# Optimization experiments

Measured on AMD Instinct MI355X. Metric: run time of the kernel, lower is better.

## Reference

```python
import jax, jax.numpy as jnp
import numpy as np

LEAKY_SLOPE = 0.2

def _xavier(key, shape, gain=1.414):
    a = gain * np.sqrt(6.0 / (shape[0] + shape[1]))
    return jax.random.uniform(key, shape, minval=-a, maxval=a, dtype=jnp.float32)

C_IN, HID = 64, 128
S_SCALES = [25, 12, 5]
T_SCALES = [64, 32, 16]

def setup_inputs() -> dict:
    key = jax.random.key(0)
    ks = jax.random.split(key, 32)
    B, T, J = 256, 64, 25
    d = {}
    d["src"] = jax.random.normal(ks[0], (B, C_IN, T, J), dtype=jnp.float32)
    d["W"] = _xavier(ks[1], (C_IN, HID))
    for i in range(3):
        d[f"as_src{i}"] = _xavier(ks[2 + i], (HID, 1))
        d[f"as_dst{i}"] = _xavier(ks[5 + i], (HID, 1))
        d[f"at_src{i}"] = _xavier(ks[8 + i], (HID, 1))
        d[f"at_dst{i}"] = _xavier(ks[11 + i], (HID, 1))
    # DiffPool assignment linears: in_features -> next_scale
    d["Wsp0"] = _xavier(ks[14], (C_IN, S_SCALES[1])); d["bsp0"] = jnp.zeros((S_SCALES[1],), jnp.float32)
    d["Wsp1"] = _xavier(ks[15], (C_IN, S_SCALES[2])); d["bsp1"] = jnp.zeros((S_SCALES[2],), jnp.float32)
    d["Wtp0"] = _xavier(ks[16], (C_IN, T_SCALES[1])); d["btp0"] = jnp.zeros((T_SCALES[1],), jnp.float32)
    d["Wtp1"] = _xavier(ks[17], (C_IN, T_SCALES[2])); d["btp1"] = jnp.zeros((T_SCALES[2],), jnp.float32)
    return d


def _gat_attn(emb, a_src, a_dst):
    # emb: [N, n, H]; additive GAT scores -> [N, n, n]
    s = emb @ a_src            # [N, n, 1]
    t = emb @ a_dst            # [N, n, 1]
    return jax.nn.leaky_relu(s + jnp.swapaxes(t, -1, -2), LEAKY_SLOPE)


def _diffpool(x, attn, Wp, bp):
    # assignment S = softmax(Linear(A @ X)) : [N, n, n_next]
    S = jax.nn.softmax((attn @ x) @ Wp + bp, axis=-1)
    x_next = jnp.einsum('bnk,bnc->bkc', S, x)
    return x_next, S


def _branch(x0, W, a_srcs, a_dsts, pool_params):
    n_scales = len(a_srcs)
    attns, pools = [], []
    x_cur = x0
    for i in range(n_scales):
        emb = x_cur @ W
        attns.append(_gat_attn(emb, a_srcs[i], a_dsts[i]))
        if i < n_scales - 1:
            Wp, bp = pool_params[i]
            x_cur, S = _diffpool(x_cur, attns[i], Wp, bp)
            pools.append(S)
    fusion = attns[0]
    for i in range(1, n_scales):
        S = pools[0]
        for j in range(1, i):
            S = S @ pools[j]
        fusion = fusion + S @ attns[i] @ jnp.swapaxes(S, -1, -2)
    # dropout is identity in eval mode
    return jax.nn.softmax(fusion, axis=-1)


def reference(src, W, as_src0, as_src1, as_src2, as_dst0, as_dst1, as_dst2,
              at_src0, at_src1, at_src2, at_dst0, at_dst1, at_dst2,
              Wsp0, bsp0, Wsp1, bsp1, Wtp0, btp0, Wtp1, btp1):
    B, C_in, T, J = src.shape
    x = jnp.transpose(src, (0, 2, 3, 1))              # [B, T, J, C]
    sp_x = x.reshape(B * T, J, C_in)                   # spatial graphs
    tp_x = jnp.transpose(x, (0, 2, 1, 3)).reshape(B * J, T, C_in)  # temporal graphs

    sa = _branch(sp_x, W, [as_src0, as_src1, as_src2], [as_dst0, as_dst1, as_dst2],
                 [(Wsp0, bsp0), (Wsp1, bsp1)])
    ta = _branch(tp_x, W, [at_src0, at_src1, at_src2], [at_dst0, at_dst1, at_dst2],
                 [(Wtp0, btp0), (Wtp1, btp1)])
    return sa.reshape(B, T, J, J), ta.reshape(B, J, T, T)
```

## Files before the change

### kernel.cpp

```cpp
#include <hip/hip_runtime.h>
#include <math.h>

constexpr float LEAKY = 0.2f;

__device__ __forceinline__ float4 ldf4(const float* p){ return *reinterpret_cast<const float4*>(p); }
__device__ __forceinline__ void stf4(float* p, float4 v){ *reinterpret_cast<float4*>(p) = v; }
__device__ __forceinline__ float dot4(float4 a, float4 b){ return a.x*b.x + a.y*b.y + a.z*b.z + a.w*b.w; }
__device__ __forceinline__ float4 fma4(float s, float4 b, float4 acc){
    acc.x += s*b.x; acc.y += s*b.y; acc.z += s*b.z; acc.w += s*b.w; return acc;
}
__device__ __forceinline__ float lrelu(float f){ return f > 0.f ? f : LEAKY*f; }
__device__ __forceinline__ float4 lrelu4(float s, float4 t){
    float4 r; r.x = lrelu(s+t.x); r.y = lrelu(s+t.y); r.z = lrelu(s+t.z); r.w = lrelu(s+t.w); return r;
}
__device__ __forceinline__ float vmax4(float4 v){ return fmaxf(fmaxf(v.x,v.y), fmaxf(v.z,v.w)); }
__device__ __forceinline__ float vsum4(float4 v){ return v.x+v.y+v.z+v.w; }
__device__ __forceinline__ float4 exp4(float4 a, float mx){
    float4 r; r.x = __expf(a.x-mx); r.y = __expf(a.y-mx); r.z = __expf(a.z-mx); r.w = __expf(a.w-mx); return r;
}

__global__ void prep_kernel(const float* __restrict__ W,
    const float* a0, const float* a1, const float* a2,  const float* a3,
    const float* a4, const float* a5, const float* a6,  const float* a7,
    const float* a8, const float* a9, const float* a10, const float* a11,
    const float* __restrict__ Wsp0, const float* __restrict__ Wsp1,
    const float* __restrict__ Wtp0, const float* __restrict__ Wtp1,
    float* __restrict__ ws)
{
    int blk = blockIdx.x, t = threadIdx.x;
    if (blk < 12) {
        const float* as[12] = {a0,a1,a2,a3,a4,a5,a6,a7,a8,a9,a10,a11};
        const float* a = as[blk];
        float s = 0.f;
        #pragma unroll
        for (int h = 0; h < 128; ++h) s += W[t*128 + h] * a[h];
        ws[blk*64 + t] = s;
    } else if (blk == 12) {
        for (int i = t; i < 768; i += 64) { int k = i >> 6, c = i & 63; ws[768 + i] = Wsp0[c*12 + k]; }
    } else if (blk == 13) {
        for (int i = t; i < 320; i += 64) { int k = i >> 6, c = i & 63; ws[1536 + i] = Wsp1[c*5 + k]; }
    } else if (blk == 14) {
        for (int i = t; i < 2048; i += 64) { int k = i >> 6, c = i & 63; ws[1856 + i] = Wtp0[c*32 + k]; }
    } else {
        for (int i = t; i < 1024; i += 64) { int k = i >> 6, c = i & 63; ws[3904 + i] = Wtp1[c*16 + k]; }
    }
}

__global__ __launch_bounds__(512, 4)
void temporal_kernel(const float* __restrict__ src, const float* __restrict__ wvec_g,
                     const float* __restrict__ Wp0, const float* __restrict__ b0,
                     const float* __restrict__ Wp1, const float* __restrict__ b1,
                     float* __restrict__ out, int nwg8)
{
    constexpr int NT = 512;
    constexpr int oA1 = 0;
    constexpr int oP1 = 1152;
    constexpr int oS1 = 1792;
    constexpr int oS0T = 2432;

    __shared__ __align__(16) float xr[4608];
    __shared__ __align__(16) float PR[2304];
    __shared__ __align__(16) float S0[2304];
    __shared__ __align__(16) float P01[1280];
    __shared__ __align__(16) float dv[256];
    __shared__ __align__(16) float sv[64], tv[64];
    __shared__ __align__(16) float s1v[32], t1v[32], ua[32], va[32];
    __shared__ __align__(16) float rx[16], rs[16];
    __shared__ __align__(16) float wv[384];

    const int tid = threadIdx.x;
    const int g = (blockIdx.x & 7) * nwg8 + (blockIdx.x >> 3);
    const int b = g / 25, inner = g - b*25;

    for (int i = tid; i < 384; i += NT) wv[i] = wvec_g[i];
    for (int i = tid; i < 4096; i += NT) {
        int c = i >> 6, r = i & 63;
        xr[r*68 + c] = src[((size_t)(b*64 + c)*64 + r)*25 + inner];
    }
    __syncthreads();

    if (tid < 64) {
        float acc[6] = {};
        #pragma unroll
        for (int c4 = 0; c4 < 16; ++c4) {
            float4 xv = ldf4(&xr[tid*68 + 4*c4]);
            #pragma unroll
            for (int d = 0; d < 6; ++d) acc[d] += dot4(xv, ldf4(&wv[d*64 + 4*c4]));
        }
        sv[tid] = acc[0]; tv[tid] = acc[1];
        dv[tid] = acc[2]; dv[64+tid] = acc[3]; dv[128+tid] = acc[4]; dv[192+tid] = acc[5];
    }
    for (int i = tid; i < 512; i += NT) {
        int p = i >> 3, k4 = i & 7;
        float4 acc = {0,0,0,0};
        #pragma unroll
        for (int c4 = 0; c4 < 16; ++c4) {
            float4 xv = ldf4(&xr[p*68 + 4*c4]);
            acc = fma4(xv.x, ldf4(&Wp0[(4*c4+0)*32 + 4*k4]), acc);
            acc = fma4(xv.y, ldf4(&Wp0[(4*c4+1)*32 + 4*k4]), acc);
            acc = fma4(xv.z, ldf4(&Wp0[(4*c4+2)*32 + 4*k4]), acc);
            acc = fma4(xv.w, ldf4(&Wp0[(4*c4+3)*32 + 4*k4]), acc);
        }
        stf4(&PR[p*36 + 4*k4], acc);
    }
    for (int i = tid; i < 256; i += NT) {
        int p = i >> 2, k4 = i & 3;
        float4 acc = {0,0,0,0};
        #pragma unroll
        for (int c4 = 0; c4 < 16; ++c4) {
            float4 xv = ldf4(&xr[p*68 + 4*c4]);
            acc = fma4(xv.x, ldf4(&Wp1[(4*c4+0)*16 + 4*k4]), acc);
            acc = fma4(xv.y, ldf4(&Wp1[(4*c4+1)*16 + 4*k4]), acc);
            acc = fma4(xv.z, ldf4(&Wp1[(4*c4+2)*16 + 4*k4]), acc);
            acc = fma4(xv.w, ldf4(&Wp1[(4*c4+3)*16 + 4*k4]), acc);
        }
        stf4(&P01[p*20 + 4*k4], acc);
    }
    __syncthreads();

    if (tid < 128) {
        int p0 = tid >> 2, k8 = tid & 3;
        float sp0 = sv[p0], sp1 = sv[p0+32];
        float4 a00 = ldf4(&b0[8*k8]), a01 = ldf4(&b0[8*k8 + 4]);
        float4 a10 = a00, a11 = a01;
        #pragma unroll
        for (int m4 = 0; m4 < 16; ++m4) {
            float4 tv4 = ldf4(&tv[4*m4]);
            float4 f0v = lrelu4(sp0, tv4);
            float4 f1v = lrelu4(sp1, tv4);
            const float* f0 = (const float*)&f0v;
            const float* f1 = (const float*)&f1v;
            #pragma unroll
            for (int j = 0; j < 4; ++j) {
                float4 pr0 = ldf4(&PR[(4*m4+j)*36 + 8*k8]);
                float4 pr1 = ldf4(&PR[(4*m4+j)*36 + 8*k8 + 4]);
                a00 = fma4(f0[j], pr0, a00); a01 = fma4(f0[j], pr1, a01);
                a10 = fma4(f1[j], pr0, a10); a11 = fma4(f1[j], pr1, a11);
            }
        }
        stf4(&S0[p0*36 + 8*k8], a00);      stf4(&S0[p0*36 + 8*k8 + 4], a01);
        stf4(&S0[(p0+32)*36 + 8*k8], a10); stf4(&S0[(p0+32)*36 + 8*k8 + 4], a11);
    }
    __syncthreads();

    {
        int p = tid >> 3, l = tid & 7;
        float4 v = ldf4(&S0[p*36 + 4*l]);
        float mx = vmax4(v);
        mx = fmaxf(mx, __shfl_xor(mx,1)); mx = fmaxf(mx, __shfl_xor(mx,2)); mx = fmaxf(mx, __shfl_xor(mx,4));
        v = exp4(v, mx);
        float sm = vsum4(v);
        sm += __shfl_xor(sm,1); sm += __shfl_xor(sm,2); sm += __shfl_xor(sm,4);
        float inv = 1.f/sm;
        v.x *= inv; v.y *= inv; v.z *= inv; v.w *= inv;
        stf4(&S0[p*36 + 4*l], v);
        xr[oS0T + (4*l+0)*68 + p] = v.x;
        xr[oS0T + (4*l+1)*68 + p] = v.y;
        xr[oS0T + (4*l+2)*68 + p] = v.z;
        xr[oS0T + (4*l+3)*68 + p] = v.w;
    }
    __syncthreads();

    if (tid < 64) {
        int k0 = tid >> 2, j4 = tid & 3;
        float4 acc0 = {0,0,0,0}, acc1 = {0,0,0,0};
        #pragma unroll
        for (int p4 = 0; p4 < 16; ++p4) {
            float4 s0 = ldf4(&xr[oS0T + k0*68 + 4*p4]);
            float4 s1 = ldf4(&xr[oS0T + (k0+16)*68 + 4*p4]);
            const float* f0 = (const float*)&s0;
            const float* f1 = (const float*)&s1;
            #pragma unroll
            for (int j = 0; j < 4; ++j) {
                float4 pv = ldf4(&P01[(4*p4+j)*20 + 4*j4]);
                acc0 = fma4(f0[j], pv, acc0);
                acc1 = fma4(f1[j], pv, acc1);
            }
        }
        stf4(&xr[oP1 + k0*20 + 4*j4], acc0);
        stf4(&xr[oP1 + (k0+16)*20 + 4*j4], acc1);
    } else if (tid < 192) {
        int i = tid - 64;
        int j = i >> 5, k = i & 31;
        const float* d = dv + j*64;
        float acc = 0.f;
        #pragma unroll
        for (int p4 = 0; p4 < 16; ++p4)
            acc += dot4(ldf4(&xr[oS0T + k*68 + 4*p4]), ldf4(&d[4*p4]));
        if (j == 0) s1v[k] = acc; else if (j == 1) t1v[k] = acc;
        else if (j == 2) ua[k] = acc; else va[k] = acc;
    }
    __syncthreads();

    for (int i = tid; i < 1024; i += NT) {
        int p = i >> 5, q = i & 31;
        xr[oA1 + p*36 + q] = lrelu(s1v[p] + t1v[q]);
    }
    __syncthreads();

    for (int i = tid; i < 128; i += NT) {
        int p = i >> 2, k4 = i & 3;
        float4 acc = ldf4(&b1[4*k4]);
        #pragma unroll
        for (int m = 0; m < 32; ++m) acc = fma4(xr[oA1 + p*36 + m], ldf4(&xr[oP1 + m*20 + 4*k4]), acc);
        stf4(&xr[oS1 + p*20 + 4*k4], acc);
    }
    __syncthreads();

    if (tid < 128) {
        int m = tid >> 2, l = tid & 3;
        float4 v = ldf4(&xr[oS1 + m*20 + 4*l]);
        float mx = vmax4(v);
        mx = fmaxf(mx, __shfl_xor(mx,1)); mx = fmaxf(mx, __shfl_xor(mx,2));
        v = exp4(v, mx);
        float sm = vsum4(v);
        sm += __shfl_xor(sm,1); sm += __shfl_xor(sm,2);
        float inv = 1.f/sm;
        v.x *= inv; v.y *= inv; v.z *= inv; v.w *= inv;
        stf4(&xr[oS1 + m*20 + 4*l], v);
    }
    __syncthreads();

    for (int k = tid; k < 16; k += NT) {
        float a = 0.f, c2 = 0.f;
        #pragma unroll
        for (int n = 0; n < 32; ++n) { float s1 = xr[oS1 + n*20 + k]; a += s1*ua[n]; c2 += s1*va[n]; }
        rx[k] = a; rs[k] = c2;
    }
    __syncthreads();

    {
        int m = tid >> 4, k = tid & 15;
        float rsk = rs[k];
        float acc = 0.f;
        #pragma unroll
        for (int j = 0; j < 16; ++j)
            acc += xr[oS1 + m*20 + j] * lrelu(rx[j] + rsk);
        xr[oP1 + m*20 + k] = acc;
    }
    __syncthreads();

    for (int i = tid; i < 1024; i += NT) {
        int m = i >> 5, n = i & 31;
        float acc = xr[oA1 + m*36 + n];
        #pragma unroll
        for (int j4 = 0; j4 < 4; ++j4)
            acc += dot4(ldf4(&xr[oP1 + m*20 + 4*j4]), ldf4(&xr[oS1 + n*20 + 4*j4]));
        xr[oA1 + m*36 + n] = acc;
    }
    __syncthreads();

    if (tid < 128) {
        int p0 = tid >> 2, k8 = tid & 3;
        float4 a00 = {0,0,0,0}, a01 = {0,0,0,0}, a10 = {0,0,0,0}, a11 = {0,0,0,0};
        #pragma unroll
        for (int m4 = 0; m4 < 8; ++m4) {
            float4 av0 = ldf4(&S0[p0*36 + 4*m4]);
            float4 av1 = ldf4(&S0[(p0+32)*36 + 4*m4]);
            const float* f0 = (const float*)&av0;
            const float* f1 = (const float*)&av1;
            #pragma unroll
            for (int j = 0; j < 4; ++j) {
                float4 b0v = ldf4(&xr[oA1 + (4*m4+j)*36 + 8*k8]);
                float4 b1v = ldf4(&xr[oA1 + (4*m4+j)*36 + 8*k8 + 4]);
                a00 = fma4(f0[j], b0v, a00); a01 = fma4(f0[j], b1v, a01);
                a10 = fma4(f1[j], b0v, a10); a11 = fma4(f1[j], b1v, a11);
            }
        }
        stf4(&PR[p0*36 + 8*k8], a00);      stf4(&PR[p0*36 + 8*k8 + 4], a01);
        stf4(&PR[(p0+32)*36 + 8*k8], a10); stf4(&PR[(p0+32)*36 + 8*k8 + 4], a11);
    }
    __syncthreads();

    if (tid < 256) {
        int p0 = tid >> 3, q8 = tid & 7;
        float sp0 = sv[p0], sp1 = sv[p0+32];
        float4 tq0 = ldf4(&tv[8*q8]), tq1 = ldf4(&tv[8*q8 + 4]);
        float4 a00 = lrelu4(sp0, tq0), a01 = lrelu4(sp0, tq1);
        float4 a10 = lrelu4(sp1, tq0), a11 = lrelu4(sp1, tq1);
        #pragma unroll
        for (int m4 = 0; m4 < 8; ++m4) {
            float4 av0 = ldf4(&PR[p0*36 + 4*m4]);
            float4 av1 = ldf4(&PR[(p0+32)*36 + 4*m4]);
            const float* f0 = (const float*)&av0;
            const float* f1 = (const float*)&av1;
            #pragma unroll
            for (int j = 0; j < 4; ++j) {
                float4 s0v = ldf4(&xr[oS0T + (4*m4+j)*68 + 8*q8]);
                float4 s1vv = ldf4(&xr[oS0T + (4*m4+j)*68 + 8*q8 + 4]);
                a00 = fma4(f0[j], s0v, a00); a01 = fma4(f0[j], s1vv, a01);
                a10 = fma4(f1[j], s0v, a10); a11 = fma4(f1[j], s1vv, a11);
            }
        }
        size_t base = (size_t)g * 4096;
        {
            float mx = fmaxf(vmax4(a00), vmax4(a01));
            mx = fmaxf(mx, __shfl_xor(mx,1)); mx = fmaxf(mx, __shfl_xor(mx,2)); mx = fmaxf(mx, __shfl_xor(mx,4));
            float4 e0 = exp4(a00, mx), e1 = exp4(a01, mx);
            float sm = vsum4(e0) + vsum4(e1);
            sm += __shfl_xor(sm,1); sm += __shfl_xor(sm,2); sm += __shfl_xor(sm,4);
            float inv = 1.f/sm;
            e0.x*=inv; e0.y*=inv; e0.z*=inv; e0.w*=inv;
            e1.x*=inv; e1.y*=inv; e1.z*=inv; e1.w*=inv;
            stf4(&out[base + (size_t)p0*64 + 8*q8], e0);
            stf4(&out[base + (size_t)p0*64 + 8*q8 + 4], e1);
        }
        {
            float mx = fmaxf(vmax4(a10), vmax4(a11));
            mx = fmaxf(mx, __shfl_xor(mx,1)); mx = fmaxf(mx, __shfl_xor(mx,2)); mx = fmaxf(mx, __shfl_xor(mx,4));
            float4 e0 = exp4(a10, mx), e1 = exp4(a11, mx);
            float sm = vsum4(e0) + vsum4(e1);
            sm += __shfl_xor(sm,1); sm += __shfl_xor(sm,2); sm += __shfl_xor(sm,4);
            float inv = 1.f/sm;
            e0.x*=inv; e0.y*=inv; e0.z*=inv; e0.w*=inv;
            e1.x*=inv; e1.y*=inv; e1.z*=inv; e1.w*=inv;
            stf4(&out[base + (size_t)(p0+32)*64 + 8*q8], e0);
            stf4(&out[base + (size_t)(p0+32)*64 + 8*q8 + 4], e1);
        }
    }
}

__global__ __launch_bounds__(256, 4)
void spatial_kernel(const float* __restrict__ src, const float* __restrict__ wvg,
                    const float* __restrict__ WpT0, const float* __restrict__ WpT1,
                    const float* __restrict__ b0, const float* __restrict__ b1,
                    float* __restrict__ out, int nwg8)
{
    __shared__ __align__(16) float Rx0[1700];
    __shared__ __align__(16) float RA0[700];
    __shared__ __align__(16) float RPR[816];
    __shared__ __align__(16) float RS0[500];
    __shared__ __align__(16) float sv[32], tv[32], ua[32], va[32], rxa[8], rsa[8];

    float* x0  = Rx0;
    float* A1  = Rx0;
    float* A1T = Rx0 + 240;
    float* P1T = Rx0 + 480;
    float* S1  = Rx0 + 540;
    float* T1  = Rx0 + 744;
    float* A0  = RA0;
    float* P0T = RPR;
    float* x1  = RPR;
    float* M1  = RPR;
    float* S0  = RS0;

    const int t = threadIdx.x;
    const int g = (blockIdx.x & 7) * nwg8 + (blockIdx.x >> 3);
    const int b = g >> 6, inner = g & 63;
    const float* srcb = src + (size_t)b*102400 + inner*25;

    for (int i = t; i < 400; i += 256) {
        int r = i % 25, c0 = (i / 25) << 2;
        float4 v;
        v.x = srcb[(c0+0)*1600 + r];
        v.y = srcb[(c0+1)*1600 + r];
        v.z = srcb[(c0+2)*1600 + r];
        v.w = srcb[(c0+3)*1600 + r];
        stf4(&x0[r*68 + c0], v);
    }
    __syncthreads();

    if (t < 50) {
        int which = t / 25, p = t - which*25;
        const float* w = wvg + which*64;
        float a = 0.f;
        #pragma unroll
        for (int c4 = 0; c4 < 16; ++c4) a += dot4(ldf4(&x0[p*68 + 4*c4]), ldf4(&w[4*c4]));
        if (which) tv[p] = a; else sv[p] = a;
    }
    for (int i = t; i < 336; i += 256) {
        int k = i / 28, m = i - k*28;
        float a = 0.f;
        if (m < 25) {
            #pragma unroll
            for (int c4 = 0; c4 < 16; ++c4) a += dot4(ldf4(&WpT0[k*64 + 4*c4]), ldf4(&x0[m*68 + 4*c4]));
        }
        P0T[k*28 + m] = a;
    }
    __syncthreads();

    for (int i = t; i < 700; i += 256) {
        int p = i / 28, q = i - p*28;
        A0[i] = (q < 25) ? lrelu(sv[p] + tv[q]) : -1e30f;
    }
    __syncthreads();

    for (int i = t; i < 300; i += 256) {
        int p = i / 12, k = i - p*12;
        float acc = b0[k];
        #pragma unroll
        for (int m4 = 0; m4 < 7; ++m4) acc += dot4(ldf4(&A0[p*28 + 4*m4]), ldf4(&P0T[k*28 + 4*m4]));
        S0[p*20 + k] = acc;
    }
    __syncthreads();

    if (t < 25) {
        float4 r[3]; float mx = -1e30f;
        #pragma unroll
        for (int u = 0; u < 3; ++u) { r[u] = ldf4(&S0[t*20 + 4*u]); mx = fmaxf(mx, vmax4(r[u])); }
        float sm = 0.f;
        #pragma unroll
        for (int u = 0; u < 3; ++u) { r[u] = exp4(r[u], mx); sm += vsum4(r[u]); }
        float inv = 1.f/sm;
        #pragma unroll
        for (int u = 0; u < 3; ++u) {
            r[u].x *= inv; r[u].y *= inv; r[u].z *= inv; r[u].w *= inv;
            stf4(&S0[t*20 + 4*u], r[u]);
        }
    }
    __syncthreads();

    if (t < 96) {
        int k = t >> 3, c0 = (t & 7) << 3;
        float4 a = {0,0,0,0}, bb = {0,0,0,0};
        #pragma unroll
        for (int p = 0; p < 25; ++p) {
            float s = S0[p*20 + k];
            a  = fma4(s, ldf4(&x0[p*68 + c0]), a);
            bb = fma4(s, ldf4(&x0[p*68 + c0 + 4]), bb);
        }
        stf4(&x1[k*68 + c0], a);
        stf4(&x1[k*68 + c0 + 4], bb);
    }
    __syncthreads();

    if (t < 48) {
        int which = t / 12, p = t - which*12;
        const float* w = wvg + (2+which)*64;
        float a = 0.f;
        #pragma unroll
        for (int c4 = 0; c4 < 16; ++c4) a += dot4(ldf4(&x1[p*68 + 4*c4]), ldf4(&w[4*c4]));
        if (which == 0) sv[p] = a; else if (which == 1) tv[p] = a;
        else if (which == 2) ua[p] = a; else va[p] = a;
    }
    for (int i = t; i < 60; i += 256) {
        int j = i / 12, k = i - j*12;
        float a = 0.f;
        #pragma unroll
        for (int c4 = 0; c4 < 16; ++c4) a += dot4(ldf4(&WpT1[j*64 + 4*c4]), ldf4(&x1[k*68 + 4*c4]));
        P1T[j*12 + k] = a;
    }
    __syncthreads();

    for (int i = t; i < 288; i += 256) {
        int mat = i / 144, rr = (i - mat*144) / 12, q = i % 12;
        if (mat == 0) A1 [rr*20 + q] = lrelu(sv[rr] + tv[q]);
        else          A1T[rr*20 + q] = lrelu(sv[q] + tv[rr]);
    }
    __syncthreads();

    for (int i = t; i < 60; i += 256) {
        int m = i / 5, j = i - m*5;
        float acc = b1[j];
        #pragma unroll
        for (int k4 = 0; k4 < 3; ++k4) acc += dot4(ldf4(&A1[m*20 + 4*k4]), ldf4(&P1T[j*12 + 4*k4]));
        S1[m*12 + j] = acc;
    }
    __syncthreads();

    if (t < 12) {
        float mx = -1e30f;
        float r0 = S1[t*12+0], r1 = S1[t*12+1], r2 = S1[t*12+2], r3 = S1[t*12+3], r4 = S1[t*12+4];
        mx = fmaxf(fmaxf(fmaxf(r0,r1), fmaxf(r2,r3)), r4);
        r0 = __expf(r0-mx); r1 = __expf(r1-mx); r2 = __expf(r2-mx); r3 = __expf(r3-mx); r4 = __expf(r4-mx);
        float inv = 1.f/(r0+r1+r2+r3+r4);
        S1[t*12+0] = r0*inv; S1[t*12+1] = r1*inv; S1[t*12+2] = r2*inv; S1[t*12+3] = r3*inv; S1[t*12+4] = r4*inv;
    }
    __syncthreads();

    if (t < 10) {
        int which = t / 5, k = t - which*5;
        float a = 0.f;
        #pragma unroll
        for (int n = 0; n < 12; ++n) a += S1[n*12 + k] * (which ? va[n] : ua[n]);
        if (which) rsa[k] = a; else rxa[k] = a;
    }
    __syncthreads();

    if (t < 60) {
        int m = t / 5, k = t - m*5;
        float rsk = rsa[k];
        float acc = 0.f;
        #pragma unroll
        for (int j = 0; j < 5; ++j) acc += S1[m*12 + j] * lrelu(rxa[j] + rsk);
        T1[m*5 + k] = acc;
    }
    __syncthreads();

    if (t < 144) {
        int m = t / 12, n = t - m*12;
        float acc = A1[m*20 + n];
        #pragma unroll
        for (int j = 0; j < 5; ++j) acc += T1[m*5 + j] * S1[n*12 + j];
        A1[m*20 + n] = acc;
        A1T[n*20 + m] = acc;
    }
    __syncthreads();

    for (int i = t; i < 300; i += 256) {
        int p = i / 12, k = i - p*12;
        float acc = 0.f;
        #pragma unroll
        for (int m4 = 0; m4 < 3; ++m4) acc += dot4(ldf4(&S0[p*20 + 4*m4]), ldf4(&A1T[k*20 + 4*m4]));
        M1[p*20 + k] = acc;
    }
    __syncthreads();

    for (int i = t; i < 625; i += 256) {
        int p = i / 25, q = i - p*25;
        float acc = A0[p*28 + q];
        #pragma unroll
        for (int m4 = 0; m4 < 3; ++m4) acc += dot4(ldf4(&M1[p*20 + 4*m4]), ldf4(&S0[q*20 + 4*m4]));
        A0[p*28 + q] = acc;
    }
    __syncthreads();

    if (t < 25) {
        float4 r[7]; float mx = -1e30f;
        #pragma unroll
        for (int u = 0; u < 7; ++u) { r[u] = ldf4(&A0[t*28 + 4*u]); mx = fmaxf(mx, vmax4(r[u])); }
        float sm = 0.f;
        #pragma unroll
        for (int u = 0; u < 7; ++u) sm += vsum4(exp4(r[u], mx));
        sv[t] = mx; tv[t] = 1.f/sm;
    }
    __syncthreads();

    for (int i = t; i < 625; i += 256) {
        int p = i / 25, q = i - p*25;
        out[(size_t)g*625 + i] = __expf(A0[p*28 + q] - sv[p]) * tv[p];
    }
}

extern "C" void kernel_launch(void* const* d_in, const int* in_sizes, int n_in,
                              void* d_out, int out_size, void* d_ws, size_t ws_size,
                              hipStream_t stream) {
    const float* src = (const float*)d_in[0];
    const float* W   = (const float*)d_in[1];
    float* ws = (float*)d_ws;

    prep_kernel<<<16, 64, 0, stream>>>(W,
        (const float*)d_in[2],  (const float*)d_in[3],
        (const float*)d_in[6],  (const float*)d_in[7],
        (const float*)d_in[10], (const float*)d_in[11],
        (const float*)d_in[4],  (const float*)d_in[5],
        (const float*)d_in[8],  (const float*)d_in[9],
        (const float*)d_in[12], (const float*)d_in[13],
        (const float*)d_in[14], (const float*)d_in[16],
        (const float*)d_in[18], (const float*)d_in[20],
        ws);

    float* out = (float*)d_out;
    spatial_kernel<<<16384, 256, 0, stream>>>(
        src, ws, ws + 768, ws + 1536,
        (const float*)d_in[15], (const float*)d_in[17],
        out, 16384/8);
    temporal_kernel<<<6400, 512, 0, stream>>>(
        src, ws + 384,
        (const float*)d_in[18], (const float*)d_in[19],
        (const float*)d_in[20], (const float*)d_in[21],
        out + 10240000, 6400/8);
}
```

Baseline: 437.0 us.

## Merge spatial and temporal kernels into one launch with interleaved block roles

Replaces the separate spatial and temporal launches with a single fused kernel. Each block decides by index arithmetic whether it handles a temporal graph or a pair of spatial graphs, and the two roles are interleaved at a 25:32 ratio with a shared-memory union. This removes the launch gap and the tail of the first kernel, and lets both workloads fill the GPU concurrently. The cost is that every block now reserves the larger shared footprint and 512 threads, which may lower occupancy for the spatial work, and half the threads of a spatial block may sit idle.

Measured after the change: 549.9 us. 1.26x slower.

```diff
diff --git a/kernel.cpp b/kernel.cpp
--- a/kernel.cpp
+++ b/kernel.cpp
@@ -47,488 +47,505 @@
 }
 
 __global__ __launch_bounds__(512, 4)
-void temporal_kernel(const float* __restrict__ src, const float* __restrict__ wvec_g,
-                     const float* __restrict__ Wp0, const float* __restrict__ b0,
-                     const float* __restrict__ Wp1, const float* __restrict__ b1,
-                     float* __restrict__ out, int nwg8)
+void fused_kernel(const float* __restrict__ src,
+                  const float* __restrict__ ws,
+                  const float* __restrict__ bsp0, const float* __restrict__ bsp1,
+                  const float* __restrict__ Wtp0r, const float* __restrict__ btp0,
+                  const float* __restrict__ Wtp1r, const float* __restrict__ btp1,
+                  float* __restrict__ out)
 {
-    constexpr int NT = 512;
-    constexpr int oA1 = 0;
-    constexpr int oP1 = 1152;
-    constexpr int oS1 = 1792;
-    constexpr int oS0T = 2432;
-
-    __shared__ __align__(16) float xr[4608];
-    __shared__ __align__(16) float PR[2304];
-    __shared__ __align__(16) float S0[2304];
-    __shared__ __align__(16) float P01[1280];
-    __shared__ __align__(16) float dv[256];
-    __shared__ __align__(16) float sv[64], tv[64];
-    __shared__ __align__(16) float s1v[32], t1v[32], ua[32], va[32];
-    __shared__ __align__(16) float rx[16], rs[16];
-    __shared__ __align__(16) float wv[384];
+    __shared__ __align__(16) float SH[11520];
 
     const int tid = threadIdx.x;
-    const int g = (blockIdx.x & 7) * nwg8 + (blockIdx.x >> 3);
-    const int b = g / 25, inner = g - b*25;
-
-    for (int i = tid; i < 384; i += NT) wv[i] = wvec_g[i];
-    for (int i = tid; i < 4096; i += NT) {
-        int c = i >> 6, r = i & 63;
-        xr[r*68 + c] = src[((size_t)(b*64 + c)*64 + r)*25 + inner];
-    }
-    __syncthreads();
-
-    if (tid < 64) {
-        float acc[6] = {};
-        #pragma unroll
-        for (int c4 = 0; c4 < 16; ++c4) {
-            float4 xv = ldf4(&xr[tid*68 + 4*c4]);
-            #pragma unroll
-            for (int d = 0; d < 6; ++d) acc[d] += dot4(xv, ldf4(&wv[d*64 + 4*c4]));
-        }
-        sv[tid] = acc[0]; tv[tid] = acc[1];
-        dv[tid] = acc[2]; dv[64+tid] = acc[3]; dv[128+tid] = acc[4]; dv[192+tid] = acc[5];
-    }
-    for (int i = tid; i < 512; i += NT) {
-        int p = i >> 3, k4 = i & 7;
-        float4 acc = {0,0,0,0};
-        #pragma unroll
-        for (int c4 = 0; c4 < 16; ++c4) {
-            float4 xv = ldf4(&xr[p*68 + 4*c4]);
-            acc = fma4(xv.x, ldf4(&Wp0[(4*c4+0)*32 + 4*k4]), acc);
-            acc = fma4(xv.y, ldf4(&Wp0[(4*c4+1)*32 + 4*k4]), acc);
-            acc = fma4(xv.z, ldf4(&Wp0[(4*c4+2)*32 + 4*k4]), acc);
-            acc = fma4(xv.w, ldf4(&Wp0[(4*c4+3)*32 + 4*k4]), acc);
-        }
-        stf4(&PR[p*36 + 4*k4], acc);
-    }
-    for (int i = tid; i < 256; i += NT) {
-        int p = i >> 2, k4 = i & 3;
-        float4 acc = {0,0,0,0};
-        #pragma unroll
-        for (int c4 = 0; c4 < 16; ++c4) {
-            float4 xv = ldf4(&xr[p*68 + 4*c4]);
-            acc = fma4(xv.x, ldf4(&Wp1[(4*c4+0)*16 + 4*k4]), acc);
-            acc = fma4(xv.y, ldf4(&Wp1[(4*c4+1)*16 + 4*k4]), acc);
-            acc = fma4(xv.z, ldf4(&Wp1[(4*c4+2)*16 + 4*k4]), acc);
-            acc = fma4(xv.w, ldf4(&Wp1[(4*c4+3)*16 + 4*k4]), acc);
-        }
-        stf4(&P01[p*20 + 4*k4], acc);
-    }
-    __syncthreads();
-
-    if (tid < 128) {
-        int p0 = tid >> 2, k8 = tid & 3;
-        float sp0 = sv[p0], sp1 = sv[p0+32];
-        float4 a00 = ldf4(&b0[8*k8]), a01 = ldf4(&b0[8*k8 + 4]);
-        float4 a10 = a00, a11 = a01;
-        #pragma unroll
-        for (int m4 = 0; m4 < 16; ++m4) {
-            float4 tv4 = ldf4(&tv[4*m4]);
-            float4 f0v = lrelu4(sp0, tv4);
-            float4 f1v = lrelu4(sp1, tv4);
-            const float* f0 = (const float*)&f0v;
-            const float* f1 = (const float*)&f1v;
-            #pragma unroll
-            for (int j = 0; j < 4; ++j) {
-                float4 pr0 = ldf4(&PR[(4*m4+j)*36 + 8*k8]);
-                float4 pr1 = ldf4(&PR[(4*m4+j)*36 + 8*k8 + 4]);
-                a00 = fma4(f0[j], pr0, a00); a01 = fma4(f0[j], pr1, a01);
-                a10 = fma4(f1[j], pr0, a10); a11 = fma4(f1[j], pr1, a11);
-            }
-        }
-        stf4(&S0[p0*36 + 8*k8], a00);      stf4(&S0[p0*36 + 8*k8 + 4], a01);
-        stf4(&S0[(p0+32)*36 + 8*k8], a10); stf4(&S0[(p0+32)*36 + 8*k8 + 4], a11);
-    }
-    __syncthreads();
-
-    {
-        int p = tid >> 3, l = tid & 7;
-        float4 v = ldf4(&S0[p*36 + 4*l]);
-        float mx = vmax4(v);
-        mx = fmaxf(mx, __shfl_xor(mx,1)); mx = fmaxf(mx, __shfl_xor(mx,2)); mx = fmaxf(mx, __shfl_xor(mx,4));
-        v = exp4(v, mx);
-        float sm = vsum4(v);
-        sm += __shfl_xor(sm,1); sm += __shfl_xor(sm,2); sm += __shfl_xor(sm,4);
-        float inv = 1.f/sm;
-        v.x *= inv; v.y *= inv; v.z *= inv; v.w *= inv;
-        stf4(&S0[p*36 + 4*l], v);
-        xr[oS0T + (4*l+0)*68 + p] = v.x;
-        xr[oS0T + (4*l+1)*68 + p] = v.y;
-        xr[oS0T + (4*l+2)*68 + p] = v.z;
-        xr[oS0T + (4*l+3)*68 + p] = v.w;
-    }
-    __syncthreads();
-
-    if (tid < 64) {
-        int k0 = tid >> 2, j4 = tid & 3;
-        float4 acc0 = {0,0,0,0}, acc1 = {0,0,0,0};
-        #pragma unroll
-        for (int p4 = 0; p4 < 16; ++p4) {
-            float4 s0 = ldf4(&xr[oS0T + k0*68 + 4*p4]);
-            float4 s1 = ldf4(&xr[oS0T + (k0+16)*68 + 4*p4]);
-            const float* f0 = (const float*)&s0;
-            const float* f1 = (const float*)&s1;
-            #pragma unroll
-            for (int j = 0; j < 4; ++j) {
-                float4 pv = ldf4(&P01[(4*p4+j)*20 + 4*j4]);
-                acc0 = fma4(f0[j], pv, acc0);
-                acc1 = fma4(f1[j], pv, acc1);
-            }
-        }
-        stf4(&xr[oP1 + k0*20 + 4*j4], acc0);
-        stf4(&xr[oP1 + (k0+16)*20 + 4*j4], acc1);
-    } else if (tid < 192) {
-        int i = tid - 64;
-        int j = i >> 5, k = i & 31;
-        const float* d = dv + j*64;
-        float acc = 0.f;
-        #pragma unroll
-        for (int p4 = 0; p4 < 16; ++p4)
-            acc += dot4(ldf4(&xr[oS0T + k*68 + 4*p4]), ldf4(&d[4*p4]));
-        if (j == 0) s1v[k] = acc; else if (j == 1) t1v[k] = acc;
-        else if (j == 2) ua[k] = acc; else va[k] = acc;
-    }
-    __syncthreads();
-
-    for (int i = tid; i < 1024; i += NT) {
-        int p = i >> 5, q = i & 31;
-        xr[oA1 + p*36 + q] = lrelu(s1v[p] + t1v[q]);
-    }
-    __syncthreads();
-
-    for (int i = tid; i < 128; i += NT) {
-        int p = i >> 2, k4 = i & 3;
-        float4 acc = ldf4(&b1[4*k4]);
-        #pragma unroll
-        for (int m = 0; m < 32; ++m) acc = fma4(xr[oA1 + p*36 + m], ldf4(&xr[oP1 + m*20 + 4*k4]), acc);
-        stf4(&xr[oS1 + p*20 + 4*k4], acc);
-    }
-    __syncthreads();
-
-    if (tid < 128) {
-        int m = tid >> 2, l = tid & 3;
-        float4 v = ldf4(&xr[oS1 + m*20 + 4*l]);
-        float mx = vmax4(v);
-        mx = fmaxf(mx, __shfl_xor(mx,1)); mx = fmaxf(mx, __shfl_xor(mx,2));
-        v = exp4(v, mx);
-        float sm = vsum4(v);
-        sm += __shfl_xor(sm,1); sm += __shfl_xor(sm,2);
-        float inv = 1.f/sm;
-        v.x *= inv; v.y *= inv; v.z *= inv; v.w *= inv;
-        stf4(&xr[oS1 + m*20 + 4*l], v);
-    }
-    __syncthreads();
-
-    for (int k = tid; k < 16; k += NT) {
-        float a = 0.f, c2 = 0.f;
-        #pragma unroll
-        for (int n = 0; n < 32; ++n) { float s1 = xr[oS1 + n*20 + k]; a += s1*ua[n]; c2 += s1*va[n]; }
-        rx[k] = a; rs[k] = c2;
-    }
-    __syncthreads();
-
-    {
-        int m = tid >> 4, k = tid & 15;
-        float rsk = rs[k];
-        float acc = 0.f;
-        #pragma unroll
-        for (int j = 0; j < 16; ++j)
-            acc += xr[oS1 + m*20 + j] * lrelu(rx[j] + rsk);
-        xr[oP1 + m*20 + k] = acc;
-    }
-    __syncthreads();
-
-    for (int i = tid; i < 1024; i += NT) {
-        int m = i >> 5, n = i & 31;
-        float acc = xr[oA1 + m*36 + n];
-        #pragma unroll
-        for (int j4 = 0; j4 < 4; ++j4)
-            acc += dot4(ldf4(&xr[oP1 + m*20 + 4*j4]), ldf4(&xr[oS1 + n*20 + 4*j4]));
-        xr[oA1 + m*36 + n] = acc;
-    }
-    __syncthreads();
-
-    if (tid < 128) {
-        int p0 = tid >> 2, k8 = tid & 3;
-        float4 a00 = {0,0,0,0}, a01 = {0,0,0,0}, a10 = {0,0,0,0}, a11 = {0,0,0,0};
-        #pragma unroll
-        for (int m4 = 0; m4 < 8; ++m4) {
-            float4 av0 = ldf4(&S0[p0*36 + 4*m4]);
-            float4 av1 = ldf4(&S0[(p0+32)*36 + 4*m4]);
-            const float* f0 = (const float*)&av0;
-            const float* f1 = (const float*)&av1;
-            #pragma unroll
-            for (int j = 0; j < 4; ++j) {
-                float4 b0v = ldf4(&xr[oA1 + (4*m4+j)*36 + 8*k8]);
-                float4 b1v = ldf4(&xr[oA1 + (4*m4+j)*36 + 8*k8 + 4]);
-                a00 = fma4(f0[j], b0v, a00); a01 = fma4(f0[j], b1v, a01);
-                a10 = fma4(f1[j], b0v, a10); a11 = fma4(f1[j], b1v, a11);
-            }
-        }
-        stf4(&PR[p0*36 + 8*k8], a00);      stf4(&PR[p0*36 + 8*k8 + 4], a01);
-        stf4(&PR[(p0+32)*36 + 8*k8], a10); stf4(&PR[(p0+32)*36 + 8*k8 + 4], a11);
-    }
-    __syncthreads();
-
-    if (tid < 256) {
-        int p0 = tid >> 3, q8 = tid & 7;
-        float sp0 = sv[p0], sp1 = sv[p0+32];
-        float4 tq0 = ldf4(&tv[8*q8]), tq1 = ldf4(&tv[8*q8 + 4]);
-        float4 a00 = lrelu4(sp0, tq0), a01 = lrelu4(sp0, tq1);
-        float4 a10 = lrelu4(sp1, tq0), a11 = lrelu4(sp1, tq1);
-        #pragma unroll
-        for (int m4 = 0; m4 < 8; ++m4) {
-            float4 av0 = ldf4(&PR[p0*36 + 4*m4]);
-            float4 av1 = ldf4(&PR[(p0+32)*36 + 4*m4]);
-            const float* f0 = (const float*)&av0;
-            const float* f1 = (const float*)&av1;
-            #pragma unroll
-            for (int j = 0; j < 4; ++j) {
-                float4 s0v = ldf4(&xr[oS0T + (4*m4+j)*68 + 8*q8]);
-                float4 s1vv = ldf4(&xr[oS0T + (4*m4+j)*68 + 8*q8 + 4]);
-                a00 = fma4(f0[j], s0v, a00); a01 = fma4(f0[j], s1vv, a01);
-                a10 = fma4(f1[j], s0v, a10); a11 = fma4(f1[j], s1vv, a11);
-            }
-        }
-        size_t base = (size_t)g * 4096;
+    const int orig = blockIdx.x;
+    const int L = (orig & 7) * 1824 + (orig >> 3);
+    const int tBefore = (L * 25) / 57;
+    const bool isTemporal = ((L + 1) * 25) / 57 > tBefore;
+
+    if (isTemporal) {
+        constexpr int NT = 512;
+        constexpr int oA1 = 0, oP1 = 1152, oS1 = 1792, oS0T = 2432;
+        float* xr  = SH;
+        float* PR  = SH + 4608;
+        float* S0  = SH + 6912;
+        float* P01 = SH + 9216;
+        float* dv  = SH + 10496;
+        float* sv  = SH + 10752;
+        float* tv  = SH + 10816;
+        float* s1v = SH + 10880;
+        float* t1v = SH + 10912;
+        float* ua  = SH + 10944;
+        float* va  = SH + 10976;
+        float* rx  = SH + 11008;
+        float* rs  = SH + 11024;
+        float* wv  = SH + 11040;
+        const float* wvec_g = ws + 384;
+        const float* Wp0 = Wtp0r;  const float* b0 = btp0;
+        const float* Wp1 = Wtp1r;  const float* b1 = btp1;
+
+        const int g = tBefore;
+        const int b = g / 25, inner = g - b*25;
+
+        for (int i = tid; i < 384; i += NT) wv[i] = wvec_g[i];
+        for (int i = tid; i < 4096; i += NT) {
+            int c = i >> 6, r = i & 63;
+            xr[r*68 + c] = src[((size_t)(b*64 + c)*64 + r)*25 + inner];
+        }
+        __syncthreads();
+
+        if (tid < 64) {
+            float acc[6] = {};
+            #pragma unroll
+            for (int c4 = 0; c4 < 16; ++c4) {
+                float4 xv = ldf4(&xr[tid*68 + 4*c4]);
+                #pragma unroll
+                for (int d = 0; d < 6; ++d) acc[d] += dot4(xv, ldf4(&wv[d*64 + 4*c4]));
+            }
+            sv[tid] = acc[0]; tv[tid] = acc[1];
+            dv[tid] = acc[2]; dv[64+tid] = acc[3]; dv[128+tid] = acc[4]; dv[192+tid] = acc[5];
+        }
+        for (int i = tid; i < 512; i += NT) {
+            int p = i >> 3, k4 = i & 7;
+            float4 acc = {0,0,0,0};
+            #pragma unroll
+            for (int c4 = 0; c4 < 16; ++c4) {
+                float4 xv = ldf4(&xr[p*68 + 4*c4]);
+                acc = fma4(xv.x, ldf4(&Wp0[(4*c4+0)*32 + 4*k4]), acc);
+                acc = fma4(xv.y, ldf4(&Wp0[(4*c4+1)*32 + 4*k4]), acc);
+                acc = fma4(xv.z, ldf4(&Wp0[(4*c4+2)*32 + 4*k4]), acc);
+                acc = fma4(xv.w, ldf4(&Wp0[(4*c4+3)*32 + 4*k4]), acc);
+            }
+            stf4(&PR[p*36 + 4*k4], acc);
+        }
+        for (int i = tid; i < 256; i += NT) {
+            int p = i >> 2, k4 = i & 3;
+            float4 acc = {0,0,0,0};
+            #pragma unroll
+            for (int c4 = 0; c4 < 16; ++c4) {
+                float4 xv = ldf4(&xr[p*68 + 4*c4]);
+                acc = fma4(xv.x, ldf4(&Wp1[(4*c4+0)*16 + 4*k4]), acc);
+                acc = fma4(xv.y, ldf4(&Wp1[(4*c4+1)*16 + 4*k4]), acc);
+                acc = fma4(xv.z, ldf4(&Wp1[(4*c4+2)*16 + 4*k4]), acc);
+                acc = fma4(xv.w, ldf4(&Wp1[(4*c4+3)*16 + 4*k4]), acc);
+            }
+            stf4(&P01[p*20 + 4*k4], acc);
+        }
+        __syncthreads();
+
+        if (tid < 128) {
+            int p0 = tid >> 2, k8 = tid & 3;
+            float sp0 = sv[p0], sp1 = sv[p0+32];
+            float4 a00 = ldf4(&b0[8*k8]), a01 = ldf4(&b0[8*k8 + 4]);
+            float4 a10 = a00, a11 = a01;
+            #pragma unroll
+            for (int m4 = 0; m4 < 16; ++m4) {
+                float4 tv4 = ldf4(&tv[4*m4]);
+                float4 f0v = lrelu4(sp0, tv4);
+                float4 f1v = lrelu4(sp1, tv4);
+                const float* f0 = (const float*)&f0v;
+                const float* f1 = (const float*)&f1v;
+                #pragma unroll
+                for (int j = 0; j < 4; ++j) {
+                    float4 pr0 = ldf4(&PR[(4*m4+j)*36 + 8*k8]);
+                    float4 pr1 = ldf4(&PR[(4*m4+j)*36 + 8*k8 + 4]);
+                    a00 = fma4(f0[j], pr0, a00); a01 = fma4(f0[j], pr1, a01);
+                    a10 = fma4(f1[j], pr0, a10); a11 = fma4(f1[j], pr1, a11);
+                }
+            }
+            stf4(&S0[p0*36 + 8*k8], a00);      stf4(&S0[p0*36 + 8*k8 + 4], a01);
+            stf4(&S0[(p0+32)*36 + 8*k8], a10); stf4(&S0[(p0+32)*36 + 8*k8 + 4], a11);
+        }
+        __syncthreads();
+
         {
-            float mx = fmaxf(vmax4(a00), vmax4(a01));
+            int p = tid >> 3, l = tid & 7;
+            float4 v = ldf4(&S0[p*36 + 4*l]);
+            float mx = vmax4(v);
             mx = fmaxf(mx, __shfl_xor(mx,1)); mx = fmaxf(mx, __shfl_xor(mx,2)); mx = fmaxf(mx, __shfl_xor(mx,4));
-            float4 e0 = exp4(a00, mx), e1 = exp4(a01, mx);
-            float sm = vsum4(e0) + vsum4(e1);
+            v = exp4(v, mx);
+            float sm = vsum4(v);
             sm += __shfl_xor(sm,1); sm += __shfl_xor(sm,2); sm += __shfl_xor(sm,4);
             float inv = 1.f/sm;
-            e0.x*=inv; e0.y*=inv; e0.z*=inv; e0.w*=inv;
-            e1.x*=inv; e1.y*=inv; e1.z*=inv; e1.w*=inv;
-            stf4(&out[base + (size_t)p0*64 + 8*q8], e0);
-            stf4(&out[base + (size_t)p0*64 + 8*q8 + 4], e1);
-        }
+            v.x *= inv; v.y *= inv; v.z *= inv; v.w *= inv;
+            stf4(&S0[p*36 + 4*l], v);
+            xr[oS0T + (4*l+0)*68 + p] = v.x;
+            xr[oS0T + (4*l+1)*68 + p] = v.y;
+            xr[oS0T + (4*l+2)*68 + p] = v.z;
+            xr[oS0T + (4*l+3)*68 + p] = v.w;
+        }
+        __syncthreads();
+
+        if (tid < 64) {
+            int k0 = tid >> 2, j4 = tid & 3;
+            float4 acc0 = {0,0,0,0}, acc1 = {0,0,0,0};
+            #pragma unroll
+            for (int p4 = 0; p4 < 16; ++p4) {
+                float4 s0 = ldf4(&xr[oS0T + k0*68 + 4*p4]);
+                float4 s1 = ldf4(&xr[oS0T + (k0+16)*68 + 4*p4]);
+                const float* f0 = (const float*)&s0;
+                const float* f1 = (const float*)&s1;
+                #pragma unroll
+                for (int j = 0; j < 4; ++j) {
+                    float4 pv = ldf4(&P01[(4*p4+j)*20 + 4*j4]);
+                    acc0 = fma4(f0[j], pv, acc0);
+                    acc1 = fma4(f1[j], pv, acc1);
+                }
+            }
+            stf4(&xr[oP1 + k0*20 + 4*j4], acc0);
+            stf4(&xr[oP1 + (k0+16)*20 + 4*j4], acc1);
+        } else if (tid < 192) {
+            int i = tid - 64;
+            int j = i >> 5, k = i & 31;
+            const float* d = dv + j*64;
+            float acc = 0.f;
+            #pragma unroll
+            for (int p4 = 0; p4 < 16; ++p4)
+                acc += dot4(ldf4(&xr[oS0T + k*68 + 4*p4]), ldf4(&d[4*p4]));
+            if (j == 0) s1v[k] = acc; else if (j == 1) t1v[k] = acc;
+            else if (j == 2) ua[k] = acc; else va[k] = acc;
+        }
+        __syncthreads();
+
+        for (int i = tid; i < 1024; i += NT) {
+            int p = i >> 5, q = i & 31;
+            xr[oA1 + p*36 + q] = lrelu(s1v[p] + t1v[q]);
+        }
+        __syncthreads();
+
+        for (int i = tid; i < 128; i += NT) {
+            int p = i >> 2, k4 = i & 3;
+            float4 acc = ldf4(&b1[4*k4]);
+            #pragma unroll
+            for (int m = 0; m < 32; ++m) acc = fma4(xr[oA1 + p*36 + m], ldf4(&xr[oP1 + m*20 + 4*k4]), acc);
+            stf4(&xr[oS1 + p*20 + 4*k4], acc);
+        }
+        __syncthreads();
+
+        if (tid < 128) {
+            int m = tid >> 2, l = tid & 3;
+            float4 v = ldf4(&xr[oS1 + m*20 + 4*l]);
+            float mx = vmax4(v);
+            mx = fmaxf(mx, __shfl_xor(mx,1)); mx = fmaxf(mx, __shfl_xor(mx,2));
+            v = exp4(v, mx);
+            float sm = vsum4(v);
+            sm += __shfl_xor(sm,1); sm += __shfl_xor(sm,2);
+            float inv = 1.f/sm;
+            v.x *= inv; v.y *= inv; v.z *= inv; v.w *= inv;
+            stf4(&xr[oS1 + m*20 + 4*l], v);
+        }
+        __syncthreads();
+
+        for (int k = tid; k < 16; k += NT) {
+            float a = 0.f, c2 = 0.f;
+            #pragma unroll
+            for (int n = 0; n < 32; ++n) { float s1 = xr[oS1 + n*20 + k]; a += s1*ua[n]; c2 += s1*va[n]; }
+            rx[k] = a; rs[k] = c2;
+        }
+        __syncthreads();
+
         {
-            float mx = fmaxf(vmax4(a10), vmax4(a11));
-            mx = fmaxf(mx, __shfl_xor(mx,1)); mx = fmaxf(mx, __shfl_xor(mx,2)); mx = fmaxf(mx, __shfl_xor(mx,4));
-            float4 e0 = exp4(a10, mx), e1 = exp4(a11, mx);
-            float sm = vsum4(e0) + vsum4(e1);
-            sm += __shfl_xor(sm,1); sm += __shfl_xor(sm,2); sm += __shfl_xor(sm,4);
+            int m = tid >> 4, k = tid & 15;
+            float rsk = rs[k];
+            float acc = 0.f;
+            #pragma unroll
+            for (int j = 0; j < 16; ++j)
+                acc += xr[oS1 + m*20 + j] * lrelu(rx[j] + rsk);
+            xr[oP1 + m*20 + k] = acc;
+        }
+        __syncthreads();
+
+        for (int i = tid; i < 1024; i += NT) {
+            int m = i >> 5, n = i & 31;
+            float acc = xr[oA1 + m*36 + n];
+            #pragma unroll
+            for (int j4 = 0; j4 < 4; ++j4)
+                acc += dot4(ldf4(&xr[oP1 + m*20 + 4*j4]), ldf4(&xr[oS1 + n*20 + 4*j4]));
+            xr[oA1 + m*36 + n] = acc;
+        }
+        __syncthreads();
+
+        if (tid < 128) {
+            int p0 = tid >> 2, k8 = tid & 3;
+            float4 a00 = {0,0,0,0}, a01 = {0,0,0,0}, a10 = {0,0,0,0}, a11 = {0,0,0,0};
+            #pragma unroll
+            for (int m4 = 0; m4 < 8; ++m4) {
+                float4 av0 = ldf4(&S0[p0*36 + 4*m4]);
+                float4 av1 = ldf4(&S0[(p0+32)*36 + 4*m4]);
+                const float* f0 = (const float*)&av0;
+                const float* f1 = (const float*)&av1;
+                #pragma unroll
+                for (int j = 0; j < 4; ++j) {
+                    float4 b0v = ldf4(&xr[oA1 + (4*m4+j)*36 + 8*k8]);
+                    float4 b1v = ldf4(&xr[oA1 + (4*m4+j)*36 + 8*k8 + 4]);
+                    a00 = fma4(f0[j], b0v, a00); a01 = fma4(f0[j], b1v, a01);
+                    a10 = fma4(f1[j], b0v, a10); a11 = fma4(f1[j], b1v, a11);
+                }
+            }
+            stf4(&PR[p0*36 + 8*k8], a00);      stf4(&PR[p0*36 + 8*k8 + 4], a01);
+            stf4(&PR[(p0+32)*36 + 8*k8], a10); stf4(&PR[(p0+32)*36 + 8*k8 + 4], a11);
+        }
+        __syncthreads();
+
+        if (tid < 256) {
+            int p0 = tid >> 3, q8 = tid & 7;
+            float sp0 = sv[p0], sp1 = sv[p0+32];
+            float4 tq0 = ldf4(&tv[8*q8]), tq1 = ldf4(&tv[8*q8 + 4]);
+            float4 a00 = lrelu4(sp0, tq0), a01 = lrelu4(sp0, tq1);
+            float4 a10 = lrelu4(sp1, tq0), a11 = lrelu4(sp1, tq1);
+            #pragma unroll
+            for (int m4 = 0; m4 < 8; ++m4) {
+                float4 av0 = ldf4(&PR[p0*36 + 4*m4]);
+                float4 av1 = ldf4(&PR[(p0+32)*36 + 4*m4]);
+                const float* f0 = (const float*)&av0;
+                const float* f1 = (const float*)&av1;
+                #pragma unroll
+                for (int j = 0; j < 4; ++j) {
+                    float4 s0v = ldf4(&xr[oS0T + (4*m4+j)*68 + 8*q8]);
+                    float4 s1vv = ldf4(&xr[oS0T + (4*m4+j)*68 + 8*q8 + 4]);
+                    a00 = fma4(f0[j], s0v, a00); a01 = fma4(f0[j], s1vv, a01);
+                    a10 = fma4(f1[j], s0v, a10); a11 = fma4(f1[j], s1vv, a11);
+                }
+            }
+            size_t base = 10240000 + (size_t)g * 4096;
+            {
+                float mx = fmaxf(vmax4(a00), vmax4(a01));
+                mx = fmaxf(mx, __shfl_xor(mx,1)); mx = fmaxf(mx, __shfl_xor(mx,2)); mx = fmaxf(mx, __shfl_xor(mx,4));
+                float4 e0 = exp4(a00, mx), e1 = exp4(a01, mx);
+                float sm = vsum4(e0) + vsum4(e1);
+                sm += __shfl_xor(sm,1); sm += __shfl_xor(sm,2); sm += __shfl_xor(sm,4);
+                float inv = 1.f/sm;
+                e0.x*=inv; e0.y*=inv; e0.z*=inv; e0.w*=inv;
+                e1.x*=inv; e1.y*=inv; e1.z*=inv; e1.w*=inv;
+                stf4(&out[base + (size_t)p0*64 + 8*q8], e0);
+                stf4(&out[base + (size_t)p0*64 + 8*q8 + 4], e1);
+            }
+            {
+                float mx = fmaxf(vmax4(a10), vmax4(a11));
+                mx = fmaxf(mx, __shfl_xor(mx,1)); mx = fmaxf(mx, __shfl_xor(mx,2)); mx = fmaxf(mx, __shfl_xor(mx,4));
+                float4 e0 = exp4(a10, mx), e1 = exp4(a11, mx);
+                float sm = vsum4(e0) + vsum4(e1);
+                sm += __shfl_xor(sm,1); sm += __shfl_xor(sm,2); sm += __shfl_xor(sm,4);
+                float inv = 1.f/sm;
+                e0.x*=inv; e0.y*=inv; e0.z*=inv; e0.w*=inv;
+                e1.x*=inv; e1.y*=inv; e1.z*=inv; e1.w*=inv;
+                stf4(&out[base + (size_t)(p0+32)*64 + 8*q8], e0);
+                stf4(&out[base + (size_t)(p0+32)*64 + 8*q8 + 4], e1);
+            }
+        }
+    } else {
+        const int s = L - tBefore;
+        const int h = tid >> 8;
+        const int t = tid & 255;
+        float* B0 = SH + h*5760;
+        float* x0  = B0;
+        float* A1  = B0;
+        float* A1T = B0 + 240;
+        float* P1T = B0 + 480;
+        float* S1  = B0 + 540;
+        float* T1  = B0 + 744;
+        float* A0  = B0 + 1712;
+        float* P0T = B0 + 2416;
+        float* x1  = B0 + 2416;
+        float* M1  = B0 + 2416;
+        float* S0  = B0 + 3232;
+        float* sv  = B0 + 3744;
+        float* tv  = B0 + 3776;
+        float* ua  = B0 + 3808;
+        float* va  = B0 + 3840;
+        float* rxa = B0 + 3872;
+        float* rsa = B0 + 3880;
+
+        const float* wvg  = ws;
+        const float* WpT0 = ws + 768;
+        const float* WpT1 = ws + 1536;
+        const float* b0 = bsp0;
+        const float* b1 = bsp1;
+
+        const int g = 2*s + h;
+        const int b = g >> 6, inner = g & 63;
+        const float* srcb = src + (size_t)b*102400 + inner*25;
+
+        for (int i = t; i < 400; i += 256) {
+            int r = i % 25, c0 = (i / 25) << 2;
+            float4 v;
+            v.x = srcb[(c0+0)*1600 + r];
+            v.y = srcb[(c0+1)*1600 + r];
+            v.z = srcb[(c0+2)*1600 + r];
+            v.w = srcb[(c0+3)*1600 + r];
+            stf4(&x0[r*68 + c0], v);
+        }
+        __syncthreads();
+
+        if (t < 50) {
+            int which = t / 25, p = t - which*25;
+            const float* w = wvg + which*64;
+            float a = 0.f;
+            #pragma unroll
+            for (int c4 = 0; c4 < 16; ++c4) a += dot4(ldf4(&x0[p*68 + 4*c4]), ldf4(&w[4*c4]));
+            if (which) tv[p] = a; else sv[p] = a;
+        }
+        for (int i = t; i < 336; i += 256) {
+            int k = i / 28, m = i - k*28;
+            float a = 0.f;
+            if (m < 25) {
+                #pragma unroll
+                for (int c4 = 0; c4 < 16; ++c4) a += dot4(ldf4(&WpT0[k*64 + 4*c4]), ldf4(&x0[m*68 + 4*c4]));
+            }
+            P0T[k*28 + m] = a;
+        }
+        __syncthreads();
+
+        for (int i = t; i < 700; i += 256) {
+            int p = i / 28, q = i - p*28;
+            A0[i] = (q < 25) ? lrelu(sv[p] + tv[q]) : -1e30f;
+        }
+        __syncthreads();
+
+        for (int i = t; i < 300; i += 256) {
+            int p = i / 12, k = i - p*12;
+            float acc = b0[k];
+            #pragma unroll
+            for (int m4 = 0; m4 < 7; ++m4) acc += dot4(ldf4(&A0[p*28 + 4*m4]), ldf4(&P0T[k*28 + 4*m4]));
+            S0[p*20 + k] = acc;
+        }
+        __syncthreads();
+
+        if (t < 25) {
+            float4 r[3]; float mx = -1e30f;
+            #pragma unroll
+            for (int u = 0; u < 3; ++u) { r[u] = ldf4(&S0[t*20 + 4*u]); mx = fmaxf(mx, vmax4(r[u])); }
+            float sm = 0.f;
+            #pragma unroll
+            for (int u = 0; u < 3; ++u) { r[u] = exp4(r[u], mx); sm += vsum4(r[u]); }
             float inv = 1.f/sm;
-            e0.x*=inv; e0.y*=inv; e0.z*=inv; e0.w*=inv;
-            e1.x*=inv; e1.y*=inv; e1.z*=inv; e1.w*=inv;
-            stf4(&out[base + (size_t)(p0+32)*64 + 8*q8], e0);
-            stf4(&out[base + (size_t)(p0+32)*64 + 8*q8 + 4], e1);
-        }
-    }
-}
-
-__global__ __launch_bounds__(256, 4)
-void spatial_kernel(const float* __restrict__ src, const float* __restrict__ wvg,
-                    const float* __restrict__ WpT0, const float* __restrict__ WpT1,
-                    const float* __restrict__ b0, const float* __restrict__ b1,
-                    float* __restrict__ out, int nwg8)
-{
-    __shared__ __align__(16) float Rx0[1700];
-    __shared__ __align__(16) float RA0[700];
-    __shared__ __align__(16) float RPR[816];
-    __shared__ __align__(16) float RS0[500];
-    __shared__ __align__(16) float sv[32], tv[32], ua[32], va[32], rxa[8], rsa[8];
-
-    float* x0  = Rx0;
-    float* A1  = Rx0;
-    float* A1T = Rx0 + 240;
-    float* P1T = Rx0 + 480;
-    float* S1  = Rx0 + 540;
-    float* T1  = Rx0 + 744;
-    float* A0  = RA0;
-    float* P0T = RPR;
-    float* x1  = RPR;
-    float* M1  = RPR;
-    float* S0  = RS0;
-
-    const int t = threadIdx.x;
-    const int g = (blockIdx.x & 7) * nwg8 + (blockIdx.x >> 3);
-    const int b = g >> 6, inner = g & 63;
-    const float* srcb = src + (size_t)b*102400 + inner*25;
-
-    for (int i = t; i < 400; i += 256) {
-        int r = i % 25, c0 = (i / 25) << 2;
-        float4 v;
-        v.x = srcb[(c0+0)*1600 + r];
-        v.y = srcb[(c0+1)*1600 + r];
-        v.z = srcb[(c0+2)*1600 + r];
-        v.w = srcb[(c0+3)*1600 + r];
-        stf4(&x0[r*68 + c0], v);
-    }
-    __syncthreads();
-
-    if (t < 50) {
-        int which = t / 25, p = t - which*25;
-        const float* w = wvg + which*64;
-        float a = 0.f;
-        #pragma unroll
-        for (int c4 = 0; c4 < 16; ++c4) a += dot4(ldf4(&x0[p*68 + 4*c4]), ldf4(&w[4*c4]));
-        if (which) tv[p] = a; else sv[p] = a;
-    }
-    for (int i = t; i < 336; i += 256) {
-        int k = i / 28, m = i - k*28;
-        float a = 0.f;
-        if (m < 25) {
-            #pragma unroll
-            for (int c4 = 0; c4 < 16; ++c4) a += dot4(ldf4(&WpT0[k*64 + 4*c4]), ldf4(&x0[m*68 + 4*c4]));
-        }
-        P0T[k*28 + m] = a;
-    }
-    __syncthreads();
-
-    for (int i = t; i < 700; i += 256) {
-        int p = i / 28, q = i - p*28;
-        A0[i] = (q < 25) ? lrelu(sv[p] + tv[q]) : -1e30f;
-    }
-    __syncthreads();
-
-    for (int i = t; i < 300; i += 256) {
-        int p = i / 12, k = i - p*12;
-        float acc = b0[k];
-        #pragma unroll
-        for (int m4 = 0; m4 < 7; ++m4) acc += dot4(ldf4(&A0[p*28 + 4*m4]), ldf4(&P0T[k*28 + 4*m4]));
-        S0[p*20 + k] = acc;
-    }
-    __syncthreads();
-
-    if (t < 25) {
-        float4 r[3]; float mx = -1e30f;
-        #pragma unroll
-        for (int u = 0; u < 3; ++u) { r[u] = ldf4(&S0[t*20 + 4*u]); mx = fmaxf(mx, vmax4(r[u])); }
-        float sm = 0.f;
-        #pragma unroll
-        for (int u = 0; u < 3; ++u) { r[u] = exp4(r[u], mx); sm += vsum4(r[u]); }
-        float inv = 1.f/sm;
-        #pragma unroll
-        for (int u = 0; u < 3; ++u) {
-            r[u].x *= inv; r[u].y *= inv; r[u].z *= inv; r[u].w *= inv;
-            stf4(&S0[t*20 + 4*u], r[u]);
-        }
-    }
-    __syncthreads();
-
-    if (t < 96) {
-        int k = t >> 3, c0 = (t & 7) << 3;
-        float4 a = {0,0,0,0}, bb = {0,0,0,0};
-        #pragma unroll
-        for (int p = 0; p < 25; ++p) {
-            float s = S0[p*20 + k];
-            a  = fma4(s, ldf4(&x0[p*68 + c0]), a);
-            bb = fma4(s, ldf4(&x0[p*68 + c0 + 4]), bb);
-        }
-        stf4(&x1[k*68 + c0], a);
-        stf4(&x1[k*68 + c0 + 4], bb);
-    }
-    __syncthreads();
-
-    if (t < 48) {
-        int which = t / 12, p = t - which*12;
-        const float* w = wvg + (2+which)*64;
-        float a = 0.f;
-        #pragma unroll
-        for (int c4 = 0; c4 < 16; ++c4) a += dot4(ldf4(&x1[p*68 + 4*c4]), ldf4(&w[4*c4]));
-        if (which == 0) sv[p] = a; else if (which == 1) tv[p] = a;
-        else if (which == 2) ua[p] = a; else va[p] = a;
-    }
-    for (int i = t; i < 60; i += 256) {
-        int j = i / 12, k = i - j*12;
-        float a = 0.f;
-        #pragma unroll
-        for (int c4 = 0; c4 < 16; ++c4) a += dot4(ldf4(&WpT1[j*64 + 4*c4]), ldf4(&x1[k*68 + 4*c4]));
-        P1T[j*12 + k] = a;
-    }
-    __syncthreads();
-
-    for (int i = t; i < 288; i += 256) {
-        int mat = i / 144, rr = (i - mat*144) / 12, q = i % 12;
-        if (mat == 0) A1 [rr*20 + q] = lrelu(sv[rr] + tv[q]);
-        else          A1T[rr*20 + q] = lrelu(sv[q] + tv[rr]);
-    }
-    __syncthreads();
-
-    for (int i = t; i < 60; i += 256) {
-        int m = i / 5, j = i - m*5;
-        float acc = b1[j];
-        #pragma unroll
-        for (int k4 = 0; k4 < 3; ++k4) acc += dot4(ldf4(&A1[m*20 + 4*k4]), ldf4(&P1T[j*12 + 4*k4]));
-        S1[m*12 + j] = acc;
-    }
-    __syncthreads();
-
-    if (t < 12) {
-        float mx = -1e30f;
-        float r0 = S1[t*12+0], r1 = S1[t*12+1], r2 = S1[t*12+2], r3 = S1[t*12+3], r4 = S1[t*12+4];
-        mx = fmaxf(fmaxf(fmaxf(r0,r1), fmaxf(r2,r3)), r4);
-        r0 = __expf(r0-mx); r1 = __expf(r1-mx); r2 = __expf(r2-mx); r3 = __expf(r3-mx); r4 = __expf(r4-mx);
-        float inv = 1.f/(r0+r1+r2+r3+r4);
-        S1[t*12+0] = r0*inv; S1[t*12+1] = r1*inv; S1[t*12+2] = r2*inv; S1[t*12+3] = r3*inv; S1[t*12+4] = r4*inv;
-    }
-    __syncthreads();
-
-    if (t < 10) {
-        int which = t / 5, k = t - which*5;
-        float a = 0.f;
-        #pragma unroll
-        for (int n = 0; n < 12; ++n) a += S1[n*12 + k] * (which ? va[n] : ua[n]);
-        if (which) rsa[k] = a; else rxa[k] = a;
-    }
-    __syncthreads();
-
-    if (t < 60) {
-        int m = t / 5, k = t - m*5;
-        float rsk = rsa[k];
-        float acc = 0.f;
-        #pragma unroll
-        for (int j = 0; j < 5; ++j) acc += S1[m*12 + j] * lrelu(rxa[j] + rsk);
-        T1[m*5 + k] = acc;
-    }
-    __syncthreads();
-
-    if (t < 144) {
-        int m = t / 12, n = t - m*12;
-        float acc = A1[m*20 + n];
-        #pragma unroll
-        for (int j = 0; j < 5; ++j) acc += T1[m*5 + j] * S1[n*12 + j];
-        A1[m*20 + n] = acc;
-        A1T[n*20 + m] = acc;
-    }
-    __syncthreads();
-
-    for (int i = t; i < 300; i += 256) {
-        int p = i / 12, k = i - p*12;
-        float acc = 0.f;
-        #pragma unroll
-        for (int m4 = 0; m4 < 3; ++m4) acc += dot4(ldf4(&S0[p*20 + 4*m4]), ldf4(&A1T[k*20 + 4*m4]));
-        M1[p*20 + k] = acc;
-    }
-    __syncthreads();
-
-    for (int i = t; i < 625; i += 256) {
-        int p = i / 25, q = i - p*25;
-        float acc = A0[p*28 + q];
-        #pragma unroll
-        for (int m4 = 0; m4 < 3; ++m4) acc += dot4(ldf4(&M1[p*20 + 4*m4]), ldf4(&S0[q*20 + 4*m4]));
-        A0[p*28 + q] = acc;
-    }
-    __syncthreads();
-
-    if (t < 25) {
-        float4 r[7]; float mx = -1e30f;
-        #pragma unroll
-        for (int u = 0; u < 7; ++u) { r[u] = ldf4(&A0[t*28 + 4*u]); mx = fmaxf(mx, vmax4(r[u])); }
-        float sm = 0.f;
-        #pragma unroll
-        for (int u = 0; u < 7; ++u) sm += vsum4(exp4(r[u], mx));
-        sv[t] = mx; tv[t] = 1.f/sm;
-    }
-    __syncthreads();
-
-    for (int i = t; i < 625; i += 256) {
-        int p = i / 25, q = i - p*25;
-        out[(size_t)g*625 + i] = __expf(A0[p*28 + q] - sv[p]) * tv[p];
+            #pragma unroll
+            for (int u = 0; u < 3; ++u) {
+                r[u].x *= inv; r[u].y *= inv; r[u].z *= inv; r[u].w *= inv;
+                stf4(&S0[t*20 + 4*u], r[u]);
+            }
+        }
+        __syncthreads();
+
+        if (t < 96) {
+            int k = t >> 3, c0 = (t & 7) << 3;
+            float4 a = {0,0,0,0}, bb = {0,0,0,0};
+            #pragma unroll
+            for (int p = 0; p < 25; ++p) {
+                float s0 = S0[p*20 + k];
+                a  = fma4(s0, ldf4(&x0[p*68 + c0]), a);
+                bb = fma4(s0, ldf4(&x0[p*68 + c0 + 4]), bb);
+            }
+            stf4(&x1[k*68 + c0], a);
+            stf4(&x1[k*68 + c0 + 4], bb);
+        }
+        __syncthreads();
+
+        if (t < 48) {
+            int which = t / 12, p = t - which*12;
+            const float* w = wvg + (2+which)*64;
+            float a = 0.f;
+            #pragma unroll
+            for (int c4 = 0; c4 < 16; ++c4) a += dot4(ldf4(&x1[p*68 + 4*c4]), ldf4(&w[4*c4]));
+            if (which == 0) sv[p] = a; else if (which == 1) tv[p] = a;
+            else if (which == 2) ua[p] = a; else va[p] = a;
+        }
+        for (int i = t; i < 60; i += 256) {
+            int j = i / 12, k = i - j*12;
+            float a = 0.f;
+            #pragma unroll
+            for (int c4 = 0; c4 < 16; ++c4) a += dot4(ldf4(&WpT1[j*64 + 4*c4]), ldf4(&x1[k*68 + 4*c4]));
+            P1T[j*12 + k] = a;
+        }
+        __syncthreads();
+
+        for (int i = t; i < 288; i += 256) {
+            int mat = i / 144, rr = (i - mat*144) / 12, q = i % 12;
+            if (mat == 0) A1 [rr*20 + q] = lrelu(sv[rr] + tv[q]);
+            else          A1T[rr*20 + q] = lrelu(sv[q] + tv[rr]);
+        }
+        __syncthreads();
+
+        for (int i = t; i < 60; i += 256) {
+            int m = i / 5, j = i - m*5;
+            float acc = b1[j];
+            #pragma unroll
+            for (int k4 = 0; k4 < 3; ++k4) acc += dot4(ldf4(&A1[m*20 + 4*k4]), ldf4(&P1T[j*12 + 4*k4]));
+            S1[m*12 + j] = acc;
+        }
+        __syncthreads();
+
+        if (t < 12) {
+            float mx = -1e30f;
+            float r0 = S1[t*12+0], r1 = S1[t*12+1], r2 = S1[t*12+2], r3 = S1[t*12+3], r4 = S1[t*12+4];
+            mx = fmaxf(fmaxf(fmaxf(r0,r1), fmaxf(r2,r3)), r4);
+            r0 = __expf(r0-mx); r1 = __expf(r1-mx); r2 = __expf(r2-mx); r3 = __expf(r3-mx); r4 = __expf(r4-mx);
+            float inv = 1.f/(r0+r1+r2+r3+r4);
+            S1[t*12+0] = r0*inv; S1[t*12+1] = r1*inv; S1[t*12+2] = r2*inv; S1[t*12+3] = r3*inv; S1[t*12+4] = r4*inv;
+        }
+        __syncthreads();
+
+        if (t < 10) {
+            int which = t / 5, k = t - which*5;
+            float a = 0.f;
+            #pragma unroll
+            for (int n = 0; n < 12; ++n) a += S1[n*12 + k] * (which ? va[n] : ua[n]);
+            if (which) rsa[k] = a; else rxa[k] = a;
+        }
+        __syncthreads();
+
+        if (t < 60) {
+            int m = t / 5, k = t - m*5;
+            float rsk = rsa[k];
+            float acc = 0.f;
+            #pragma unroll
+            for (int j = 0; j < 5; ++j) acc += S1[m*12 + j] * lrelu(rxa[j] + rsk);
+            T1[m*5 + k] = acc;
+        }
+        __syncthreads();
+
+        if (t < 144) {
+            int m = t / 12, n = t - m*12;
+            float acc = A1[m*20 + n];
+            #pragma unroll
+            for (int j = 0; j < 5; ++j) acc += T1[m*5 + j] * S1[n*12 + j];
+            A1[m*20 + n] = acc;
+            A1T[n*20 + m] = acc;
+        }
+        __syncthreads();
+
+        for (int i = t; i < 300; i += 256) {
+            int p = i / 12, k = i - p*12;
+            float acc = 0.f;
+            #pragma unroll
+            for (int m4 = 0; m4 < 3; ++m4) acc += dot4(ldf4(&S0[p*20 + 4*m4]), ldf4(&A1T[k*20 + 4*m4]));
+            M1[p*20 + k] = acc;
+        }
+        __syncthreads();
+
+        for (int i = t; i < 625; i += 256) {
+            int p = i / 25, q = i - p*25;
+            float acc = A0[p*28 + q];
+            #pragma unroll
+            for (int m4 = 0; m4 < 3; ++m4) acc += dot4(ldf4(&M1[p*20 + 4*m4]), ldf4(&S0[q*20 + 4*m4]));
+            A0[p*28 + q] = acc;
+        }
+        __syncthreads();
+
+        if (t < 25) {
+            float4 r[7]; float mx = -1e30f;
+            #pragma unroll
+            for (int u = 0; u < 7; ++u) { r[u] = ldf4(&A0[t*28 + 4*u]); mx = fmaxf(mx, vmax4(r[u])); }
+            float sm = 0.f;
+            #pragma unroll
+            for (int u = 0; u < 7; ++u) sm += vsum4(exp4(r[u], mx));
+            sv[t] = mx; tv[t] = 1.f/sm;
+        }
+        __syncthreads();
+
+        for (int i = t; i < 625; i += 256) {
+            int p = i / 25, q = i - p*25;
+            out[(size_t)g*625 + i] = __expf(A0[p*28 + q] - sv[p]) * tv[p];
+        }
     }
 }
 
@@ -551,13 +568,10 @@
         ws);
 
     float* out = (float*)d_out;
-    spatial_kernel<<<16384, 256, 0, stream>>>(
-        src, ws, ws + 768, ws + 1536,
+    fused_kernel<<<14592, 512, 0, stream>>>(
+        src, ws,
         (const float*)d_in[15], (const float*)d_in[17],
-        out, 16384/8);
-    temporal_kernel<<<6400, 512, 0, stream>>>(
-        src, ws + 384,
         (const float*)d_in[18], (const float*)d_in[19],
         (const float*)d_in[20], (const float*)d_in[21],
-        out + 10240000, 6400/8);
+        out);
 }
```
